# Performance work log

Hardware: AMD Instinct MI355X
Metric: run time of the kernel (lower is better)

Reference implementation:

```python
import jax, jax.numpy as jnp
import numpy as np

B, L, C, H, W = 4, 32, 16, 64, 64


def setup_inputs() -> dict:
    key = jax.random.key(0)
    k1, k2 = jax.random.split(key)
    # small flows so warps stay mostly local (realistic optical-flow magnitudes)
    flows = jax.random.normal(k1, (B, L, 2, H, W), dtype=jnp.float32) * 0.1
    images = jax.random.normal(k2, (B, L, C, H, W), dtype=jnp.float32)
    return {"flows": flows, "images": images}


def _wrap(x):
    # wrap_coord: map into [-1, 1) periodically (jnp.mod with positive divisor is non-negative)
    return jnp.mod(x + 1.0, 2.0) - 1.0


def _bilinear(images, ix, iy):
    # images: [B, K, C, H, W]; ix, iy: [B, K, H, W] pixel-space coords
    Bb, K, Cc, Hh, Ww = images.shape
    x0 = jnp.floor(ix).astype(jnp.int32)
    y0 = jnp.floor(iy).astype(jnp.int32)
    x1 = x0 + 1
    y1 = y0 + 1
    wx1 = ix - x0.astype(ix.dtype)
    wy1 = iy - y0.astype(iy.dtype)
    wx0 = 1.0 - wx1
    wy0 = 1.0 - wy1
    flat = images.reshape(Bb, K, Cc, Hh * Ww)

    def gat(xi, yi):
        valid = ((xi >= 0) & (xi < Ww) & (yi >= 0) & (yi < Hh)).astype(images.dtype)
        idx = (jnp.clip(yi, 0, Hh - 1) * Ww + jnp.clip(xi, 0, Ww - 1)).reshape(Bb, K, 1, Hh * Ww)
        v = jnp.take_along_axis(flat, idx, axis=3).reshape(Bb, K, Cc, Hh, Ww)
        return v * valid[:, :, None]  # zero padding outside image

    return ((wx0 * wy0)[:, :, None] * gat(x0, y0)
            + (wx1 * wy0)[:, :, None] * gat(x1, y0)
            + (wx0 * wy1)[:, :, None] * gat(x0, y1)
            + (wx1 * wy1)[:, :, None] * gat(x1, y1))


def _forward(flows, images):
    Bb, Ll, Cc, Hh, Ww = images.shape
    # cumulative flow, computed in fp32 then cast back (matches torch.cumsum(...).to(dtype))
    cum = jnp.cumsum(flows.astype(jnp.float32), axis=1).astype(flows.dtype)  # [B,L,2,H,W]
    bx = (jnp.arange(Ww, dtype=jnp.float32) + 0.5) * (2.0 / Ww) - 1.0
    by = (jnp.arange(Hh, dtype=jnp.float32) + 0.5) * (2.0 / Hh) - 1.0
    base_x = jnp.broadcast_to(bx[None, :], (Hh, Ww))
    base_y = jnp.broadcast_to(by[:, None], (Hh, Ww))
    # mask[t, k] = 1 iff k <= t (causal accumulation over past frames)
    mask = jnp.tril(jnp.ones((Ll, Ll), dtype=images.dtype))

    def step(carry, inp):
        cum_t, mrow = inp  # cum_t: [B,2,H,W], mrow: [L]
        rel = cum_t[:, None] - cum  # [B,L,2,H,W] = flow_t - flow_k
        gx = _wrap(base_x + rel[:, :, 0])
        gy = _wrap(base_y + rel[:, :, 1])
        ix = (gx + 1.0) * 0.5 * Ww - 0.5
        iy = (gy + 1.0) * 0.5 * Hh - 0.5
        warped = _bilinear(images, ix, iy)  # [B,L,C,H,W]
        out_t = jnp.einsum('blchw,l->bchw', warped, mrow)
        return carry, out_t

    _, ys = jax.lax.scan(step, None, (jnp.moveaxis(cum, 1, 0), mask))
    return jnp.moveaxis(ys, 0, 1)  # [B,L,C,H,W]


def reference(flows, images):
    return _forward(flows, images)
```

## Files before the change

### kernel.cpp

```cpp
#include <hip/hip_runtime.h>


constexpr int BN = 4, LN = 32, CN = 16, HWn = 4096;
constexpr int FRAME = CN * HWn;
constexpr int PW = 66, PCELLS = PW * PW;
constexpr int CHUNK_B = PCELLS * 16;
constexpr size_t TIMG_BYTES = (size_t)BN * LN * 2 * CHUNK_B;
constexpr size_t CUM_BYTES  = (size_t)BN * LN * HWn * 2 * 4;

__global__ __launch_bounds__(1024) void prep_pad(
        const float* __restrict__ img, float4* __restrict__ timg) {
    const int f = blockIdx.x >> 1, g = blockIdx.x & 1;
    const float* src = img + (size_t)f * FRAME + g * (8 * HWn);
    float4* dst = timg + (size_t)blockIdx.x * PCELLS;
    for (int q = threadIdx.x; q < PCELLS; q += 1024) {
        const int y = q / PW, x = q - y * PW;
        union { float4 f4; _Float16 h[8]; } cell;
        if (y >= 1 && y <= 64 && x >= 1 && x <= 64) {
            const int p = ((y - 1) << 6) + (x - 1);
#pragma unroll
            for (int c = 0; c < 8; ++c)
                cell.h[c] = (_Float16)src[c * HWn + p];
        } else {
            cell.f4 = make_float4(0.f, 0.f, 0.f, 0.f);
        }
        dst[q] = cell.f4;
    }
}

__global__ __launch_bounds__(256) void prep_cum(
        const float* __restrict__ flows, float2* __restrict__ cum) {
    const int b = blockIdx.x >> 4;
    const int p = ((blockIdx.x & 15) << 8) + threadIdx.x;
    const float* fl = flows + (size_t)b * (LN * 2 * HWn) + p;
    float cx = 0.f, cy = 0.f;
    for (int l = 0; l < LN; ++l) {
        cx += fl[(2 * l) * HWn];
        cy += fl[(2 * l + 1) * HWn];
        cum[(size_t)(b * LN + l) * HWn + p] = make_float2(cx, cy);
    }
}

__device__ __forceinline__ void px_step(const float4* __restrict__ fr,
                                        float2 ct, float2 ck,
                                        float bx, float by,
                                        float* __restrict__ acc) {
    const float vx = (bx + (ct.x - ck.x)) + 1.0f;
    const float vy = (by + (ct.y - ck.y)) + 1.0f;
    const float ux = vx * 0.5f, uy = vy * 0.5f;
    const float fx = ux - floorf(ux);
    const float fy = uy - floorf(uy);
    const float ixp = fmaf(fx, 64.0f, 0.5f);
    const float iyp = fmaf(fy, 64.0f, 0.5f);
    const float xf = floorf(ixp), yf = floorf(iyp);
    const int x0p = (int)xf, y0p = (int)yf;
    const float wx1 = ixp - xf, wy1 = iyp - yf;
    const float wx0 = 1.0f - wx1, wy0 = 1.0f - wy1;
    const float w00 = wx0 * wy0, w10 = wx1 * wy0;
    const float w01 = wx0 * wy1, w11 = wx1 * wy1;
    const int i00 = y0p * PW + x0p;
    union { float4 f4; _Float16 h[8]; } g00, g10, g01, g11;
    g00.f4 = fr[i00];
    g10.f4 = fr[i00 + 1];
    g01.f4 = fr[i00 + PW];
    g11.f4 = fr[i00 + PW + 1];
#pragma unroll
    for (int c = 0; c < 8; ++c) {
        float s = fmaf((float)g00.h[c], w00, acc[c]);
        s = fmaf((float)g10.h[c], w10, s);
        s = fmaf((float)g01.h[c], w01, s);
        acc[c] = fmaf((float)g11.h[c], w11, s);
    }
}

__global__ __launch_bounds__(1024, 4) void gsps_lds(
        const float2* __restrict__ cum,
        const char* __restrict__ timg,
        float* __restrict__ out) {
    extern __shared__ char smem[];
    const int bid = blockIdx.x;
    const int xs  = bid & 7;
    const int b   = xs >> 1;
    const int pxh = xs & 1;
    const int seq = bid >> 3;
    const int pair = seq & 15;
    const int chh  = seq >> 4;
    const int tid  = threadIdx.x;
    const int t1 = 31 - pair;
    const int t2 = pair;

    const int px0 = (pxh << 11) + tid;
    const int px1 = px0 + 1024;
    const float bx0 = ((float)(px0 & 63) + 0.5f) * 0.03125f - 1.0f;
    const float by0 = ((float)(px0 >> 6) + 0.5f) * 0.03125f - 1.0f;
    const float bx1 = ((float)(px1 & 63) + 0.5f) * 0.03125f - 1.0f;
    const float by1 = ((float)(px1 >> 6) + 0.5f) * 0.03125f - 1.0f;

    const float2* cb = cum + (size_t)b * (LN * HWn);
    const size_t chunk0 = ((size_t)b * LN * 2 + chh) * CHUNK_B;
    const unsigned wbase = (unsigned)(tid & ~63) << 4;

#define STAGE(KK, BUF) do {                                                   \
    const char* gsrc = timg + chunk0 + (size_t)(KK) * (2 * CHUNK_B);          \
    char* lbase = smem + (BUF) * CHUNK_B + wbase;                             \
    _Pragma("unroll")                                                         \
    for (int j = 0; j < 4; ++j) {                                             \
        __builtin_amdgcn_global_load_lds(                                     \
            (const __attribute__((address_space(1))) void*)                  \
                (gsrc + (j * 16384 + tid * 16)),                              \
            (__attribute__((address_space(3))) void*)(lbase + j * 16384),    \
            16, 0, 0);                                                        \
    }                                                                         \
    if (tid < PCELLS - 4096) {                     \
        __builtin_amdgcn_global_load_lds(                                     \
            (const __attribute__((address_space(1))) void*)                  \
                (gsrc + (65536 + tid * 16)),                                  \
            (__attribute__((address_space(3))) void*)(lbase + 65536),        \
            16, 0, 0);                                                        \
    }                                                                         \
} while (0)

    float acc0[8] = {0}, acc1[8] = {0};
    float2 ct0 = make_float2(0.f, 0.f), ct1 = ct0;
    float2 ckp0 = cb[px0], ckp1 = cb[px1];

    STAGE(0, 0);

    for (int i = 0; i < 33; ++i) {
        const bool ph2 = (i > t1);
        const int k = ph2 ? (i - t1 - 1) : i;
        const int t = ph2 ? t2 : t1;

        __syncthreads();
        if (i < 32) {
            const int kn = (i + 1 > t1) ? (i - t1) : (i + 1);
            STAGE(kn, (i + 1) & 1);
        }

        const float2 ck0 = ckp0, ck1 = ckp1;
        if (i < 32) {
            const int kn = (i + 1 > t1) ? (i - t1) : (i + 1);
            ckp0 = cb[kn * HWn + px0];
            ckp1 = cb[kn * HWn + px1];
        }
        if (k == 0) {
            ct0 = cb[t * HWn + px0];
            ct1 = cb[t * HWn + px1];
#pragma unroll
            for (int c = 0; c < 8; ++c) { acc0[c] = 0.f; acc1[c] = 0.f; }
        }
        const float4* fr = (const float4*)(smem + (i & 1) * CHUNK_B);
        px_step(fr, ct0, ck0, bx0, by0, acc0);
        px_step(fr, ct1, ck1, bx1, by1, acc1);

        if (k == t) {
            float* op = out + ((size_t)(b * LN + t) * CN + chh * 8) * HWn;
#pragma unroll
            for (int c = 0; c < 8; ++c) {
                op[c * HWn + px0] = acc0[c];
                op[c * HWn + px1] = acc1[c];
            }
        }
    }
#undef STAGE
}

__global__ __launch_bounds__(256) void gsps_slow(
        const float* __restrict__ flows,
        const float* __restrict__ img,
        float* __restrict__ out) {
    const int bi = blockIdx.x;
    const int tile = bi & 15;
    const int rest = bi >> 4;
    const int t = 31 - (rest & 31);
    const int b = rest >> 5;
    const int p = (tile << 8) + threadIdx.x;
    const int h = p >> 6, w = p & 63;
    const float base_x = ((float)w + 0.5f) * 0.03125f - 1.0f;
    const float base_y = ((float)h + 0.5f) * 0.03125f - 1.0f;
    const float* fl = flows + (size_t)b * (LN * 2 * HWn) + p;

    float ctx = 0.f, cty = 0.f;
    for (int j = 0; j <= t; ++j) { ctx += fl[(2*j)*HWn]; cty += fl[(2*j+1)*HWn]; }

    float acc[16];
#pragma unroll
    for (int c = 0; c < 16; ++c) acc[c] = 0.f;

    float ckx = 0.f, cky = 0.f;
    for (int k = 0; k <= t; ++k) {
        ckx += fl[(2*k)*HWn]; cky += fl[(2*k+1)*HWn];
        float vx = (base_x + (ctx - ckx)) + 1.0f;
        float vy = (base_y + (cty - cky)) + 1.0f;
        float mx = vx - 2.0f * floorf(vx * 0.5f);
        float my = vy - 2.0f * floorf(vy * 0.5f);
        const float ix = ((mx - 1.0f) + 1.0f) * 32.0f - 0.5f;
        const float iy = ((my - 1.0f) + 1.0f) * 32.0f - 0.5f;
        const float x0f = floorf(ix), y0f = floorf(iy);
        const int x0 = (int)x0f, y0 = (int)y0f;
        const float wx1 = ix - x0f, wy1 = iy - y0f;
        const float wx0 = 1.0f - wx1, wy0 = 1.0f - wy1;
        const int x1 = x0 + 1, y1 = y0 + 1;
        const float fx0 = (x0 >= 0) ? 1.0f : 0.0f;
        const float fx1 = (x1 <= 63) ? 1.0f : 0.0f;
        const float fy0 = (y0 >= 0) ? 1.0f : 0.0f;
        const float fy1 = (y1 <= 63) ? 1.0f : 0.0f;
        const int x0c = (x0 < 0) ? 0 : x0, x1c = (x1 > 63) ? 63 : x1;
        const int y0c = (y0 < 0) ? 0 : y0, y1c = (y1 > 63) ? 63 : y1;
        const float w00 = (wx0*wy0)*(fx0*fy0), w10 = (wx1*wy0)*(fx1*fy0);
        const float w01 = (wx0*wy1)*(fx0*fy1), w11 = (wx1*wy1)*(fx1*fy1);
        const float* frm = img + (size_t)(b * LN + k) * FRAME;
        const int i00 = (y0c<<6)+x0c, i10 = (y0c<<6)+x1c;
        const int i01 = (y1c<<6)+x0c, i11 = (y1c<<6)+x1c;
#pragma unroll
        for (int c = 0; c < 16; ++c) {
            const float* pl = frm + c * HWn;
            acc[c] += ((w00*pl[i00] + w10*pl[i10]) + w01*pl[i01]) + w11*pl[i11];
        }
    }
    float* op = out + (size_t)(b * LN + t) * FRAME + p;
#pragma unroll
    for (int c = 0; c < 16; ++c) op[c * HWn] = acc[c];
}

extern "C" void kernel_launch(void* const* d_in, const int* in_sizes, int n_in,
                              void* d_out, int out_size, void* d_ws, size_t ws_size,
                              hipStream_t stream) {
    const float* flows  = (const float*)d_in[0];
    const float* images = (const float*)d_in[1];
    float* out = (float*)d_out;

    bool fast = (ws_size >= TIMG_BYTES + CUM_BYTES);
    if (fast) {
        hipError_t e = hipFuncSetAttribute(
            reinterpret_cast<const void*>(&gsps_lds),
            hipFuncAttributeMaxDynamicSharedMemorySize, 2 * CHUNK_B);
        if (e != hipSuccess) fast = false;
    }
    if (fast) {
        float4* timg = (float4*)d_ws;
        float2* cumw = (float2*)((char*)d_ws + TIMG_BYTES);
        prep_pad<<<BN * LN * 2, 1024, 0, stream>>>(images, timg);
        prep_cum<<<BN * 16, 256, 0, stream>>>(flows, cumw);
        gsps_lds<<<256, 1024, 2 * CHUNK_B, stream>>>(
            cumw, (const char*)timg, out);
    } else {
        gsps_slow<<<BN * LN * 16, 256, 0, stream>>>(flows, images, out);
    }
}
```

Before: 91.44 us.

## Split channels into four 4-channel fp16 groups with smaller LDS frame tiles

Repacks the padded fp16 image into four channel groups of 4 (8-byte cells) instead of two groups of 8 (16-byte cells), halving the per-block LDS frame buffer. Each block now runs 512 threads covering 4 pixels each for 4 channels, and the grid doubles to 512 blocks. The aim is more resident blocks per CU and more blocks to fill the GPU. The cost is that the warp coordinate and weight math and the cumulative-flow loads are repeated for twice as many channel groups, and each LDS gather now moves 8 bytes instead of 16.

```diff
diff --git a/kernel.cpp b/kernel.cpp
--- a/kernel.cpp
+++ b/kernel.cpp
@@ -4,27 +4,27 @@
 constexpr int BN = 4, LN = 32, CN = 16, HWn = 4096;
 constexpr int FRAME = CN * HWn;
 constexpr int PW = 66, PCELLS = PW * PW;
-constexpr int CHUNK_B = PCELLS * 16;
-constexpr size_t TIMG_BYTES = (size_t)BN * LN * 2 * CHUNK_B;
+constexpr int CH_B = PCELLS * 8;
+constexpr size_t TIMG_BYTES = (size_t)BN * LN * 4 * CH_B;
 constexpr size_t CUM_BYTES  = (size_t)BN * LN * HWn * 2 * 4;
 
-__global__ __launch_bounds__(1024) void prep_pad(
-        const float* __restrict__ img, float4* __restrict__ timg) {
-    const int f = blockIdx.x >> 1, g = blockIdx.x & 1;
-    const float* src = img + (size_t)f * FRAME + g * (8 * HWn);
-    float4* dst = timg + (size_t)blockIdx.x * PCELLS;
-    for (int q = threadIdx.x; q < PCELLS; q += 1024) {
+__global__ __launch_bounds__(512) void prep_pad(
+        const float* __restrict__ img, uint2* __restrict__ timg) {
+    const int f = blockIdx.x >> 2, q4 = blockIdx.x & 3;
+    const float* src = img + (size_t)f * FRAME + q4 * (4 * HWn);
+    uint2* dst = timg + (size_t)blockIdx.x * PCELLS;
+    for (int q = threadIdx.x; q < PCELLS; q += 512) {
         const int y = q / PW, x = q - y * PW;
-        union { float4 f4; _Float16 h[8]; } cell;
+        union { uint2 u2; _Float16 h[4]; } cell;
         if (y >= 1 && y <= 64 && x >= 1 && x <= 64) {
             const int p = ((y - 1) << 6) + (x - 1);
 #pragma unroll
-            for (int c = 0; c < 8; ++c)
+            for (int c = 0; c < 4; ++c)
                 cell.h[c] = (_Float16)src[c * HWn + p];
         } else {
-            cell.f4 = make_float4(0.f, 0.f, 0.f, 0.f);
-        }
-        dst[q] = cell.f4;
+            cell.u2 = make_uint2(0u, 0u);
+        }
+        dst[q] = cell.u2;
     }
 }
 
@@ -41,10 +41,10 @@
     }
 }
 
-__device__ __forceinline__ void px_step(const float4* __restrict__ fr,
-                                        float2 ct, float2 ck,
-                                        float bx, float by,
-                                        float* __restrict__ acc) {
+__device__ __forceinline__ void px_step4(const uint2* __restrict__ fr,
+                                         float2 ct, float2 ck,
+                                         float bx, float by,
+                                         float* __restrict__ acc) {
     const float vx = (bx + (ct.x - ck.x)) + 1.0f;
     const float vy = (by + (ct.y - ck.y)) + 1.0f;
     const float ux = vx * 0.5f, uy = vy * 0.5f;
@@ -59,13 +59,13 @@
     const float w00 = wx0 * wy0, w10 = wx1 * wy0;
     const float w01 = wx0 * wy1, w11 = wx1 * wy1;
     const int i00 = y0p * PW + x0p;
-    union { float4 f4; _Float16 h[8]; } g00, g10, g01, g11;
-    g00.f4 = fr[i00];
-    g10.f4 = fr[i00 + 1];
-    g01.f4 = fr[i00 + PW];
-    g11.f4 = fr[i00 + PW + 1];
-#pragma unroll
-    for (int c = 0; c < 8; ++c) {
+    union { uint2 u2; _Float16 h[4]; } g00, g10, g01, g11;
+    g00.u2 = fr[i00];
+    g10.u2 = fr[i00 + 1];
+    g01.u2 = fr[i00 + PW];
+    g11.u2 = fr[i00 + PW + 1];
+#pragma unroll
+    for (int c = 0; c < 4; ++c) {
         float s = fmaf((float)g00.h[c], w00, acc[c]);
         s = fmaf((float)g10.h[c], w10, s);
         s = fmaf((float)g01.h[c], w01, s);
@@ -73,56 +73,57 @@
     }
 }
 
-__global__ __launch_bounds__(1024, 4) void gsps_lds(
+__global__ __launch_bounds__(512, 4) void gsps_lds(
         const float2* __restrict__ cum,
         const char* __restrict__ timg,
         float* __restrict__ out) {
     extern __shared__ char smem[];
     const int bid = blockIdx.x;
-    const int xs  = bid & 7;
-    const int b   = xs >> 1;
-    const int pxh = xs & 1;
-    const int seq = bid >> 3;
-    const int pair = seq & 15;
-    const int chh  = seq >> 4;
+    const int b    = bid & 3;
+    const int chq  = (bid >> 2) & 3;
+    const int pair = (bid >> 4) & 15;
+    const int pxh  = bid >> 8;
     const int tid  = threadIdx.x;
     const int t1 = 31 - pair;
     const int t2 = pair;
 
-    const int px0 = (pxh << 11) + tid;
-    const int px1 = px0 + 1024;
-    const float bx0 = ((float)(px0 & 63) + 0.5f) * 0.03125f - 1.0f;
-    const float by0 = ((float)(px0 >> 6) + 0.5f) * 0.03125f - 1.0f;
-    const float bx1 = ((float)(px1 & 63) + 0.5f) * 0.03125f - 1.0f;
-    const float by1 = ((float)(px1 >> 6) + 0.5f) * 0.03125f - 1.0f;
-
-    const float2* cb = cum + (size_t)b * (LN * HWn);
-    const size_t chunk0 = ((size_t)b * LN * 2 + chh) * CHUNK_B;
+    const int px_0 = (pxh << 11) + tid;
+    const float bxA = ((float)(px_0 & 63) + 0.5f) * 0.03125f - 1.0f;
+    const float byA = ((float)(px_0 >> 6) + 0.5f) * 0.03125f - 1.0f;
+    const float bxB = ((float)((px_0 + 512) & 63) + 0.5f) * 0.03125f - 1.0f;
+    const float byB = ((float)((px_0 + 512) >> 6) + 0.5f) * 0.03125f - 1.0f;
+    const float bxC = ((float)((px_0 + 1024) & 63) + 0.5f) * 0.03125f - 1.0f;
+    const float byC = ((float)((px_0 + 1024) >> 6) + 0.5f) * 0.03125f - 1.0f;
+    const float bxD = ((float)((px_0 + 1536) & 63) + 0.5f) * 0.03125f - 1.0f;
+    const float byD = ((float)((px_0 + 1536) >> 6) + 0.5f) * 0.03125f - 1.0f;
+
+    const float2* cb = cum + (size_t)b * (LN * HWn) + px_0;
+    const size_t chunk0 = ((size_t)b * LN * 4 + chq) * CH_B;
     const unsigned wbase = (unsigned)(tid & ~63) << 4;
 
 #define STAGE(KK, BUF) do {                                                   \
-    const char* gsrc = timg + chunk0 + (size_t)(KK) * (2 * CHUNK_B);          \
-    char* lbase = smem + (BUF) * CHUNK_B + wbase;                             \
+    const char* gsrc = timg + chunk0 + (size_t)(KK) * (4 * CH_B);             \
+    char* lbase = smem + (BUF) * CH_B + wbase;                                \
     _Pragma("unroll")                                                         \
     for (int j = 0; j < 4; ++j) {                                             \
         __builtin_amdgcn_global_load_lds(                                     \
             (const __attribute__((address_space(1))) void*)                  \
-                (gsrc + (j * 16384 + tid * 16)),                              \
-            (__attribute__((address_space(3))) void*)(lbase + j * 16384),    \
+                (gsrc + (j * 8192 + tid * 16)),                               \
+            (__attribute__((address_space(3))) void*)(lbase + j * 8192),     \
             16, 0, 0);                                                        \
     }                                                                         \
-    if (tid < PCELLS - 4096) {                     \
+    if (tid < (CH_B - 32768) / 16) {                 \
         __builtin_amdgcn_global_load_lds(                                     \
             (const __attribute__((address_space(1))) void*)                  \
-                (gsrc + (65536 + tid * 16)),                                  \
-            (__attribute__((address_space(3))) void*)(lbase + 65536),        \
+                (gsrc + (32768 + tid * 16)),                                  \
+            (__attribute__((address_space(3))) void*)(lbase + 32768),        \
             16, 0, 0);                                                        \
     }                                                                         \
 } while (0)
 
-    float acc0[8] = {0}, acc1[8] = {0};
-    float2 ct0 = make_float2(0.f, 0.f), ct1 = ct0;
-    float2 ckp0 = cb[px0], ckp1 = cb[px1];
+    float accA[4] = {0}, accB[4] = {0}, accC[4] = {0}, accD[4] = {0};
+    float2 ctA = make_float2(0.f, 0.f), ctB = ctA, ctC = ctA, ctD = ctA;
+    float2 ckpA = cb[0], ckpB = cb[512], ckpC = cb[1024], ckpD = cb[1536];
 
     STAGE(0, 0);
 
@@ -137,28 +138,34 @@
             STAGE(kn, (i + 1) & 1);
         }
 
-        const float2 ck0 = ckp0, ck1 = ckp1;
+        const float2 ckA = ckpA, ckB = ckpB, ckC = ckpC, ckD = ckpD;
         if (i < 32) {
             const int kn = (i + 1 > t1) ? (i - t1) : (i + 1);
-            ckp0 = cb[kn * HWn + px0];
-            ckp1 = cb[kn * HWn + px1];
+            const float2* cn = cb + kn * HWn;
+            ckpA = cn[0]; ckpB = cn[512]; ckpC = cn[1024]; ckpD = cn[1536];
         }
         if (k == 0) {
-            ct0 = cb[t * HWn + px0];
-            ct1 = cb[t * HWn + px1];
-#pragma unroll
-            for (int c = 0; c < 8; ++c) { acc0[c] = 0.f; acc1[c] = 0.f; }
-        }
-        const float4* fr = (const float4*)(smem + (i & 1) * CHUNK_B);
-        px_step(fr, ct0, ck0, bx0, by0, acc0);
-        px_step(fr, ct1, ck1, bx1, by1, acc1);
+            const float2* cl = cb + t * HWn;
+            ctA = cl[0]; ctB = cl[512]; ctC = cl[1024]; ctD = cl[1536];
+#pragma unroll
+            for (int c = 0; c < 4; ++c)
+                { accA[c] = 0.f; accB[c] = 0.f; accC[c] = 0.f; accD[c] = 0.f; }
+        }
+        const uint2* fr = (const uint2*)(smem + (i & 1) * CH_B);
+        px_step4(fr, ctA, ckA, bxA, byA, accA);
+        px_step4(fr, ctB, ckB, bxB, byB, accB);
+        px_step4(fr, ctC, ckC, bxC, byC, accC);
+        px_step4(fr, ctD, ckD, bxD, byD, accD);
 
         if (k == t) {
-            float* op = out + ((size_t)(b * LN + t) * CN + chh * 8) * HWn;
-#pragma unroll
-            for (int c = 0; c < 8; ++c) {
-                op[c * HWn + px0] = acc0[c];
-                op[c * HWn + px1] = acc1[c];
+            float* op = out + ((size_t)(b * LN + t) * CN + chq * 4) * HWn
+                      + px_0;
+#pragma unroll
+            for (int c = 0; c < 4; ++c) {
+                op[c * HWn         ] = accA[c];
+                op[c * HWn + 512   ] = accB[c];
+                op[c * HWn + 1024  ] = accC[c];
+                op[c * HWn + 1536  ] = accD[c];
             }
         }
     }
@@ -234,15 +241,15 @@
     if (fast) {
         hipError_t e = hipFuncSetAttribute(
             reinterpret_cast<const void*>(&gsps_lds),
-            hipFuncAttributeMaxDynamicSharedMemorySize, 2 * CHUNK_B);
+            hipFuncAttributeMaxDynamicSharedMemorySize, 2 * CH_B);
         if (e != hipSuccess) fast = false;
     }
     if (fast) {
-        float4* timg = (float4*)d_ws;
+        uint2* timg = (uint2*)d_ws;
         float2* cumw = (float2*)((char*)d_ws + TIMG_BYTES);
-        prep_pad<<<BN * LN * 2, 1024, 0, stream>>>(images, timg);
+        prep_pad<<<BN * LN * 4, 512, 0, stream>>>(images, timg);
         prep_cum<<<BN * 16, 256, 0, stream>>>(flows, cumw);
-        gsps_lds<<<256, 1024, 2 * CHUNK_B, stream>>>(
+        gsps_lds<<<512, 512, 2 * CH_B, stream>>>(
             cumw, (const char*)timg, out);
     } else {
         gsps_slow<<<BN * LN * 16, 256, 0, stream>>>(flows, images, out);
```

Result: faster. 88.64 us (-3.1%).
